# Kernel optimization log

Hardware: AMD Instinct MI355X
Metric: run time of the kernel (lower is better)

The kernel has to match this reference:

```python
import jax, jax.numpy as jnp
import numpy as np

DIM = 4096
N_HEADS = 32
N_KV = 8
HEAD_DIM = DIM // N_HEADS  # 128
ROPE_THETA = 10000.0


def setup_inputs() -> dict:
    key = jax.random.key(0)
    ks = jax.random.split(key, 5)
    B, S = 1, 2048
    x = jax.random.normal(ks[0], (B, S, DIM), jnp.float32)
    wq = jax.random.normal(ks[1], (N_HEADS * HEAD_DIM, DIM), jnp.float32) * 0.02
    wk = jax.random.normal(ks[2], (N_KV * HEAD_DIM, DIM), jnp.float32) * 0.02
    wv = jax.random.normal(ks[3], (N_KV * HEAD_DIM, DIM), jnp.float32) * 0.02
    wo = jax.random.normal(ks[4], (DIM, DIM), jnp.float32) * 0.02
    # precomputed RoPE frequencies: angle[t, i] = t / theta^(2i/head_dim)
    inv_freq = 1.0 / (ROPE_THETA ** (jnp.arange(0, HEAD_DIM, 2, dtype=jnp.float32) / HEAD_DIM))
    t = jnp.arange(S, dtype=jnp.float32)
    angles = jnp.outer(t, inv_freq)  # [S, HEAD_DIM/2]
    return {"x": x, "wq": wq, "wk": wk, "wv": wv, "wo": wo,
            "freqs_cos": jnp.cos(angles), "freqs_sin": jnp.sin(angles)}


def _apply_rope(v, cos, sin):
    # v: [B, S, H, HEAD_DIM]; cos/sin: [S, HEAD_DIM/2]
    # mirrors torch view_as_complex on (..., hd/2, 2): even idx = real, odd idx = imag
    vr = v.reshape(*v.shape[:-1], HEAD_DIM // 2, 2)
    xr, xi = vr[..., 0], vr[..., 1]
    c = cos[None, :, None, :]
    s = sin[None, :, None, :]
    out_r = xr * c - xi * s
    out_i = xr * s + xi * c
    return jnp.stack([out_r, out_i], axis=-1).reshape(v.shape)


def reference(x, wq, wk, wv, wo, freqs_cos, freqs_sin):
    B, S, _ = x.shape
    rep = N_HEADS // N_KV
    q = (x @ wq.T).reshape(B, S, N_HEADS, HEAD_DIM)
    k = (x @ wk.T).reshape(B, S, N_KV, HEAD_DIM)
    v = (x @ wv.T).reshape(B, S, N_KV, HEAD_DIM)
    q = _apply_rope(q, freqs_cos, freqs_sin)
    k = _apply_rope(k, freqs_cos, freqs_sin)
    # native GQA: group query heads per kv head instead of materializing repeated KV
    qg = q.reshape(B, S, N_KV, rep, HEAD_DIM)
    scale = 1.0 / jnp.sqrt(jnp.asarray(HEAD_DIM, jnp.float32))
    scores = jnp.einsum('bqkrd,bskd->bkrqs', qg, k) * scale  # [B, n_kv, rep, S, S]
    causal = jnp.tril(jnp.ones((S, S), bool))
    scores = jnp.where(causal, scores, -jnp.inf)
    probs = jax.nn.softmax(scores, axis=-1)
    out = jnp.einsum('bkrqs,bskd->bqkrd', probs, v).reshape(B, S, DIM)
    return out @ wo.T
```

## Files before the change

### kernel.cpp

```cpp
#include <hip/hip_runtime.h>
#include <cstdint>

typedef __attribute__((ext_vector_type(8))) __bf16 bf16x8;
typedef __attribute__((ext_vector_type(4))) float  f32x4;
typedef __attribute__((ext_vector_type(8))) unsigned short ushort8;

#define DIM 4096
#define SEQ 2048
#define NH  32
#define NKV 8
#define HD  128

__device__ __forceinline__ float b2f(unsigned short u) {
  union { unsigned int i; float f; } v; v.i = ((unsigned int)u) << 16; return v.f;
}
__device__ __forceinline__ unsigned short f2b(float f) {
  union { float f; unsigned int i; } v; v.f = f;
  unsigned int r = v.i + 0x7fffu + ((v.i >> 16) & 1u);
  return (unsigned short)(r >> 16);
}

__device__ __forceinline__ void gl_lds16(const void* g, void* l) {
  __builtin_amdgcn_global_load_lds(
      (const __attribute__((address_space(1))) void*)(uintptr_t)g,
      (__attribute__((address_space(3))) void*)(uintptr_t)l,
      16, 0, 0);
}

__global__ __launch_bounds__(256) void f32_to_bf16(const float* __restrict__ src,
                                                   unsigned short* __restrict__ dst, int n) {
  const int i = (blockIdx.x * 256 + threadIdx.x) * 8;
  if (i >= n) return;
  const float4 a = *(const float4*)(src + i);
  const float4 b = *(const float4*)(src + i + 4);
  ushort8 o;
  o[0] = f2b(a.x); o[1] = f2b(a.y); o[2] = f2b(a.z); o[3] = f2b(a.w);
  o[4] = f2b(b.x); o[5] = f2b(b.y); o[6] = f2b(b.z); o[7] = f2b(b.w);
  *(ushort8*)(dst + i) = o;
}

template <bool OUT_F32>
__global__ __launch_bounds__(256) void gemm_bt(const unsigned short* __restrict__ A,
                                               const unsigned short* __restrict__ B,
                                               void* __restrict__ Cv,
                                               int M, int N, int K) {
  __shared__ __align__(16) unsigned short As[128 * 32];
  __shared__ __align__(16) unsigned short Bs[128 * 32];
  const int n0   = blockIdx.x * 128;
  const int m0   = blockIdx.y * 128;
  const int tid  = threadIdx.x;
  const int w    = tid >> 6;
  const int lane = tid & 63;
  const int quad = lane >> 4;
  const int l15  = lane & 15;
  const int wm   = (w & 1) * 64;
  const int wn   = (w >> 1) * 64;

  const f32x4 fzero = {0.f, 0.f, 0.f, 0.f};
  f32x4 acc[4][4];
#pragma unroll
  for (int i = 0; i < 4; ++i)
#pragma unroll
    for (int j = 0; j < 4; ++j) acc[i][j] = fzero;

  const int srow = lane >> 2;
  const int scol = (lane & 3) * 8;

  for (int k0 = 0; k0 < K; k0 += 32) {
    __syncthreads();
#pragma unroll
    for (int cc = 0; cc < 2; ++cc) {
      const int c   = w * 2 + cc;
      const int row = c * 16 + srow;
      gl_lds16(A + (size_t)(m0 + row) * K + k0 + scol, (char*)As + c * 1024);
      gl_lds16(B + (size_t)(n0 + row) * K + k0 + scol, (char*)Bs + c * 1024);
    }
    __syncthreads();

    bf16x8 af[4], bfr[4];
#pragma unroll
    for (int i = 0; i < 4; ++i) {
      af[i]  = *(const bf16x8*)(As + (wm + i * 16 + l15) * 32 + quad * 8);
      bfr[i] = *(const bf16x8*)(Bs + (wn + i * 16 + l15) * 32 + quad * 8);
    }
#pragma unroll
    for (int i = 0; i < 4; ++i)
#pragma unroll
      for (int j = 0; j < 4; ++j)
        acc[i][j] = __builtin_amdgcn_mfma_f32_16x16x32_bf16(af[i], bfr[j], acc[i][j], 0, 0, 0);
  }

#pragma unroll
  for (int i = 0; i < 4; ++i)
#pragma unroll
    for (int j = 0; j < 4; ++j) {
      const int m = m0 + wm + i * 16 + quad * 4;
      const int n = n0 + wn + j * 16 + l15;
      if (OUT_F32) {
        float* cp = (float*)Cv + (size_t)m * N + n;
#pragma unroll
        for (int r = 0; r < 4; ++r) cp[(size_t)r * N] = acc[i][j][r];
      } else {
        unsigned short* cp = (unsigned short*)Cv + (size_t)m * N + n;
#pragma unroll
        for (int r = 0; r < 4; ++r) cp[(size_t)r * N] = f2b(acc[i][j][r]);
      }
    }
}

template <bool OUT_F32>
__global__ __launch_bounds__(512, 2) void gemm256(const unsigned short* __restrict__ A,
                                                  const unsigned short* __restrict__ B,
                                                  void* __restrict__ Cv,
                                                  int M, int N, int K) {
  __shared__ __align__(16) unsigned short As[2][256 * 64];
  __shared__ __align__(16) unsigned short Bs[2][256 * 64];

  const int n0   = blockIdx.x * 256;
  const int m0   = blockIdx.y * 256;
  const int tid  = threadIdx.x;
  const int w    = tid >> 6;
  const int lane = tid & 63;
  const int quad = lane >> 4;
  const int l15  = lane & 15;
  const int wm   = (w >> 2) * 128;
  const int wn   = (w & 3) * 64;

  const int srow = lane >> 3;
  const int sgr  = (lane & 7) ^ srow;
  const unsigned short* aS = A + (size_t)(m0 + srow) * K + sgr * 8;
  const unsigned short* bS = B + (size_t)(n0 + srow) * K + sgr * 8;

  const int gr0 = ((quad)     ^ (l15 & 7)) * 8;
  const int gr1 = ((quad + 4) ^ (l15 & 7)) * 8;

  const f32x4 fzero = {0.f, 0.f, 0.f, 0.f};
  f32x4 acc[8][4];
#pragma unroll
  for (int i = 0; i < 8; ++i)
#pragma unroll
    for (int j = 0; j < 4; ++j) acc[i][j] = fzero;

  const int NT = K >> 6;

#pragma unroll
  for (int tp = 0; tp < 2; ++tp)
#pragma unroll
    for (int i = 0; i < 4; ++i) {
      const int c = w * 4 + i;
      gl_lds16(aS + (size_t)c * 8 * K + tp * 64, (char*)As[tp] + c * 1024);
      gl_lds16(bS + (size_t)c * 8 * K + tp * 64, (char*)Bs[tp] + c * 1024);
    }

  for (int t = 0; t < NT; ++t) {
    const unsigned short* Ab = As[t & 1] + (wm + l15) * 64;
    const unsigned short* Bb = Bs[t & 1] + (wn + l15) * 64;

    if (t + 2 < NT) asm volatile("s_waitcnt vmcnt(8)" ::: "memory");
    else            asm volatile("s_waitcnt vmcnt(0)" ::: "memory");
    __builtin_amdgcn_s_barrier();
    __builtin_amdgcn_sched_barrier(0);

    bf16x8 af[8][2], bfr[4][2];
#pragma unroll
    for (int mf = 0; mf < 8; ++mf) {
      af[mf][0] = *(const bf16x8*)(Ab + mf * 1024 + gr0);
      af[mf][1] = *(const bf16x8*)(Ab + mf * 1024 + gr1);
    }
#pragma unroll
    for (int nf = 0; nf < 4; ++nf) {
      bfr[nf][0] = *(const bf16x8*)(Bb + nf * 1024 + gr0);
      bfr[nf][1] = *(const bf16x8*)(Bb + nf * 1024 + gr1);
    }

    __builtin_amdgcn_s_setprio(1);
#pragma unroll
    for (int ks = 0; ks < 2; ++ks)
#pragma unroll
      for (int mf = 0; mf < 4; ++mf)
#pragma unroll
        for (int nf = 0; nf < 4; ++nf)
          acc[mf][nf] = __builtin_amdgcn_mfma_f32_16x16x32_bf16(af[mf][ks], bfr[nf][ks],
                                                                acc[mf][nf], 0, 0, 0);
    __builtin_amdgcn_s_setprio(0);

    asm volatile("s_waitcnt lgkmcnt(0)" ::: "memory");
    __builtin_amdgcn_sched_barrier(0);
    __builtin_amdgcn_s_barrier();

    if (t + 2 < NT) {
      const int koff = (t + 2) * 64;
      unsigned short* Ad = As[t & 1];
      unsigned short* Bd = Bs[t & 1];
#pragma unroll
      for (int i = 0; i < 4; ++i) {
        const int c = w * 4 + i;
        gl_lds16(aS + (size_t)c * 8 * K + koff, (char*)Ad + c * 1024);
        gl_lds16(bS + (size_t)c * 8 * K + koff, (char*)Bd + c * 1024);
      }
    }

    __builtin_amdgcn_s_setprio(1);
#pragma unroll
    for (int ks = 0; ks < 2; ++ks)
#pragma unroll
      for (int mf = 4; mf < 8; ++mf)
#pragma unroll
        for (int nf = 0; nf < 4; ++nf)
          acc[mf][nf] = __builtin_amdgcn_mfma_f32_16x16x32_bf16(af[mf][ks], bfr[nf][ks],
                                                                acc[mf][nf], 0, 0, 0);
    __builtin_amdgcn_s_setprio(0);
  }

#pragma unroll
  for (int mf = 0; mf < 8; ++mf)
#pragma unroll
    for (int nf = 0; nf < 4; ++nf) {
      const int m = m0 + wm + mf * 16 + quad * 4;
      const int n = n0 + wn + nf * 16 + l15;
      if (OUT_F32) {
        float* cp = (float*)Cv + (size_t)m * N + n;
#pragma unroll
        for (int r = 0; r < 4; ++r) cp[(size_t)r * N] = acc[mf][nf][r];
      } else {
        unsigned short* cp = (unsigned short*)Cv + (size_t)m * N + n;
#pragma unroll
        for (int r = 0; r < 4; ++r) cp[(size_t)r * N] = f2b(acc[mf][nf][r]);
      }
    }
}

__global__ void rope_kernel(unsigned short* __restrict__ q, int qstride,
                            unsigned short* __restrict__ k, int kstride,
                            const float* __restrict__ Ct, const float* __restrict__ St) {
  const int idx = blockIdx.x * 256 + threadIdx.x;
  const int total = SEQ * (NH * 64 + NKV * 64);
  if (idx >= total) return;
  const int s = idx / 2560;
  const int r = idx - s * 2560;
  unsigned short* base;
  int i;
  if (r < NH * 64) {
    const int h = r >> 6; i = r & 63;
    base = q + (size_t)s * qstride + h * HD + 2 * i;
  } else {
    const int r2 = r - NH * 64; const int h = r2 >> 6; i = r2 & 63;
    base = k + (size_t)s * kstride + h * HD + 2 * i;
  }
  const float c  = Ct[s * 64 + i];
  const float sn = St[s * 64 + i];
  const float xr = b2f(base[0]);
  const float xi = b2f(base[1]);
  base[0] = f2b(xr * c - xi * sn);
  base[1] = f2b(xr * sn + xi * c);
}

__global__ __launch_bounds__(256) void transpose_v(const unsigned short* __restrict__ v,
                                                   int vstride,
                                                   unsigned short* __restrict__ vt) {
  __shared__ unsigned short tile[64][72];
  const int bs = blockIdx.x;
  const int bd = blockIdx.y;
  const int t  = threadIdx.x;
  const int r  = t >> 2;
  const int c0 = (t & 3) * 16;
  const unsigned short* src = v + (size_t)(bs * 64 + r) * vstride + bd * 64 + c0;
#pragma unroll
  for (int i = 0; i < 2; ++i) {
    ushort8 d = *(const ushort8*)(src + i * 8);
#pragma unroll
    for (int e = 0; e < 8; ++e) tile[r][c0 + i * 8 + e] = d[e];
  }
  __syncthreads();
  unsigned short* dst = vt + (size_t)(bd * 64 + r) * SEQ + bs * 64 + c0;
#pragma unroll
  for (int i = 0; i < 2; ++i) {
    ushort8 o;
#pragma unroll
    for (int e = 0; e < 8; ++e) o[e] = tile[c0 + i * 8 + e][r];
    *(ushort8*)(dst + i * 8) = o;
  }
}

__global__ __launch_bounds__(256) void attn_kernel(const unsigned short* __restrict__ Q, int qstride,
                                                   const unsigned short* __restrict__ K, int kstride,
                                                   const unsigned short* __restrict__ VT,
                                                   unsigned short* __restrict__ O) {
  const int bid  = blockIdx.x;
  const int h    = bid & 31;
  const int pr   = bid >> 5;
  const int g    = h >> 2;
  const int tid  = threadIdx.x;
  const int w    = tid >> 6;
  const int lane = tid & 63;
  const int quad = lane >> 4;
  const int l15  = lane & 15;

  __shared__ __align__(16) unsigned short Ks[64 * 128];
  __shared__ __align__(16) unsigned short Vs[128 * 64];
  __shared__ __align__(16) unsigned short Ps[4][32 * 64];

  const float scale = 0.08838834764831845f;
  const f32x4 fzero = {0.f, 0.f, 0.f, 0.f};

  bf16x8 onesf;
#pragma unroll
  for (int e = 0; e < 8; ++e) onesf[e] = (__bf16)1.0f;

  const int ks_row = (lane >> 4);
  const int ks_q   = (lane & 15);
  const int vs_row = (lane >> 3);
  const int vs_q   = (lane & 7) ^ (lane >> 3);

  unsigned short* pw = Ps[w];

  for (int phase = 0; phase < 2; ++phase) {
    const int qt    = phase ? (15 - pr) : pr;
    const int qrow0 = qt * 128 + w * 32;

    bf16x8 qf[2][4];
#pragma unroll
    for (int gq = 0; gq < 2; ++gq) {
      const unsigned short* qb = Q + (size_t)(qrow0 + gq * 16 + l15) * qstride + h * HD + quad * 8;
#pragma unroll
      for (int c = 0; c < 4; ++c) qf[gq][c] = *(const bf16x8*)(qb + c * 32);
    }

    f32x4 oa[2][8];
    f32x4 ls[2];
#pragma unroll
    for (int gq = 0; gq < 2; ++gq) {
      ls[gq] = fzero;
#pragma unroll
      for (int i = 0; i < 8; ++i) oa[gq][i] = fzero;
    }

    const int n_tiles = 2 * qt + 2;

    for (int kt = 0; kt < n_tiles; ++kt) {
      const int kv0 = kt * 64;
      __syncthreads();
#pragma unroll
      for (int cc = 0; cc < 4; ++cc) {
        const int c = w * 4 + cc;
        {
          const int row = c * 4 + ks_row;
          const int qch = ks_q ^ (row & 15);
          gl_lds16(K + (size_t)(kv0 + row) * kstride + g * HD + qch * 8, (char*)Ks + c * 1024);
        }
        {
          const int row = c * 8 + vs_row;
          gl_lds16(VT + (size_t)(g * HD + row) * SEQ + kv0 + vs_q * 8, (char*)Vs + c * 1024);
        }
      }
      __syncthreads();

      f32x4 s[2][4];
#pragma unroll
      for (int gq = 0; gq < 2; ++gq)
#pragma unroll
        for (int ks = 0; ks < 4; ++ks) s[gq][ks] = fzero;
#pragma unroll
      for (int c = 0; c < 4; ++c)
#pragma unroll
        for (int ks = 0; ks < 4; ++ks) {
          const int row = ks * 16 + l15;
          const int p   = (c * 4 + quad) ^ l15;
          bf16x8 kf = *(const bf16x8*)(Ks + row * 128 + p * 8);
          s[0][ks] = __builtin_amdgcn_mfma_f32_16x16x32_bf16(qf[0][c], kf, s[0][ks], 0, 0, 0);
          s[1][ks] = __builtin_amdgcn_mfma_f32_16x16x32_bf16(qf[1][c], kf, s[1][ks], 0, 0, 0);
        }

#pragma unroll
      for (int gq = 0; gq < 2; ++gq)
#pragma unroll
        for (int r = 0; r < 4; ++r) {
          const int qrow = qrow0 + gq * 16 + quad * 4 + r;
          const int prow = gq * 16 + quad * 4 + r;
#pragma unroll
          for (int ks = 0; ks < 4; ++ks) {
            const float ex = __expf(s[gq][ks][r] * scale);
            const float e  = (kv0 + ks * 16 + l15 <= qrow) ? ex : 0.f;
            const int qc = ks * 2 + (l15 >> 3);
            const int p  = qc ^ (prow & 7);
            pw[prow * 64 + p * 8 + (l15 & 7)] = f2b(e);
          }
        }

#pragma unroll
      for (int ki = 0; ki < 2; ++ki) {
        bf16x8 pf[2];
#pragma unroll
        for (int gq = 0; gq < 2; ++gq) {
          const int row = gq * 16 + l15;
          const int p   = (ki * 4 + quad) ^ (l15 & 7);
          pf[gq] = *(const bf16x8*)(pw + row * 64 + p * 8);
        }
        ls[0] = __builtin_amdgcn_mfma_f32_16x16x32_bf16(pf[0], onesf, ls[0], 0, 0, 0);
        ls[1] = __builtin_amdgcn_mfma_f32_16x16x32_bf16(pf[1], onesf, ls[1], 0, 0, 0);
#pragma unroll
        for (int nt = 0; nt < 8; ++nt) {
          const int vrow = nt * 16 + l15;
          const int p    = (ki * 4 + quad) ^ (l15 & 7);
          bf16x8 vf = *(const bf16x8*)(Vs + vrow * 64 + p * 8);
          oa[0][nt] = __builtin_amdgcn_mfma_f32_16x16x32_bf16(pf[0], vf, oa[0][nt], 0, 0, 0);
          oa[1][nt] = __builtin_amdgcn_mfma_f32_16x16x32_bf16(pf[1], vf, oa[1][nt], 0, 0, 0);
        }
      }
    }

#pragma unroll
    for (int gq = 0; gq < 2; ++gq)
#pragma unroll
      for (int r = 0; r < 4; ++r) {
        const float inv = 1.f / ls[gq][r];
        const int qrow = qrow0 + gq * 16 + quad * 4 + r;
        unsigned short* orow = O + (size_t)qrow * DIM + h * HD;
#pragma unroll
        for (int nt = 0; nt < 8; ++nt) orow[nt * 16 + l15] = f2b(oa[gq][nt][r] * inv);
      }
  }
}

extern "C" void kernel_launch(void* const* d_in, const int* in_sizes, int n_in,
                              void* d_out, int out_size, void* d_ws, size_t ws_size,
                              hipStream_t stream) {
  const float* x  = (const float*)d_in[0];
  const float* wq = (const float*)d_in[1];
  const float* wk = (const float*)d_in[2];
  const float* wv = (const float*)d_in[3];
  const float* wo = (const float*)d_in[4];
  const float* fc = (const float*)d_in[5];
  const float* fs = (const float*)d_in[6];
  float* outp = (float*)d_out;

  const dim3 blk(256);
  const size_t M1 = 1024 * 1024;
  const int nx  = SEQ * DIM;
  const int nqw = DIM * DIM;
  const int nkw = NKV * HD * DIM;
  const int total = SEQ * (NH * 64 + NKV * 64);

  const size_t fused_elems = (8 + 24 + 12 + 2 + 8) * M1;

  if (ws_size >= fused_elems * 2) {
    unsigned short* xb   = (unsigned short*)d_ws;
    unsigned short* wbuf = xb   + 8  * M1;
    unsigned short* qkv  = wbuf + 24 * M1;
    unsigned short* vtb  = qkv  + 12 * M1;
    unsigned short* aob  = vtb  + 2  * M1;

    f32_to_bf16<<<dim3(nx  / 2048), blk, 0, stream>>>(x,  xb, nx);
    f32_to_bf16<<<dim3(nqw / 2048), blk, 0, stream>>>(wq, wbuf, nqw);
    f32_to_bf16<<<dim3(nkw / 2048), blk, 0, stream>>>(wk, wbuf + 16 * M1, nkw);
    f32_to_bf16<<<dim3(nkw / 2048), blk, 0, stream>>>(wv, wbuf + 20 * M1, nkw);

    gemm256<false><<<dim3(6144 / 256, SEQ / 256), dim3(512), 0, stream>>>(xb, wbuf, qkv,
                                                                          SEQ, 6144, DIM);

    rope_kernel<<<dim3((total + 255) / 256), blk, 0, stream>>>(qkv, 6144, qkv + 4096, 6144, fc, fs);
    transpose_v<<<dim3(SEQ / 64, 1024 / 64), blk, 0, stream>>>(qkv + 5120, 6144, vtb);
    attn_kernel<<<dim3(256), blk, 0, stream>>>(qkv, 6144, qkv + 4096, 6144, vtb, aob);

    f32_to_bf16<<<dim3(nqw / 2048), blk, 0, stream>>>(wo, wbuf, nqw);
    gemm_bt<true><<<dim3(DIM / 128, SEQ / 128), blk, 0, stream>>>(aob, wbuf, outp, SEQ, DIM, DIM);
  } else {
    unsigned short* xb   = (unsigned short*)d_ws;
    unsigned short* wbuf = xb   + 8  * M1;
    unsigned short* qb   = wbuf + 16 * M1;
    unsigned short* kvb  = qb   + 8  * M1;
    unsigned short* vtb  = kvb  + 4  * M1;
    unsigned short* aob  = vtb  + 2  * M1;

    f32_to_bf16<<<dim3(nx  / 2048), blk, 0, stream>>>(x,  xb, nx);
    f32_to_bf16<<<dim3(nqw / 2048), blk, 0, stream>>>(wq, wbuf, nqw);
    gemm_bt<false><<<dim3(DIM / 128, SEQ / 128), blk, 0, stream>>>(xb, wbuf, qb, SEQ, DIM, DIM);

    f32_to_bf16<<<dim3(nkw / 2048), blk, 0, stream>>>(wk, wbuf, nkw);
    f32_to_bf16<<<dim3(nkw / 2048), blk, 0, stream>>>(wv, wbuf + 4 * M1, nkw);
    gemm_bt<false><<<dim3(2048 / 128, SEQ / 128), blk, 0, stream>>>(xb, wbuf, kvb, SEQ, 2048, DIM);

    rope_kernel<<<dim3((total + 255) / 256), blk, 0, stream>>>(qb, 4096, kvb, 2048, fc, fs);
    transpose_v<<<dim3(SEQ / 64, 1024 / 64), blk, 0, stream>>>(kvb + 1024, 2048, vtb);
    attn_kernel<<<dim3(256), blk, 0, stream>>>(qb, 4096, kvb, 2048, vtb, aob);

    f32_to_bf16<<<dim3(nqw / 2048), blk, 0, stream>>>(wo, wbuf, nqw);
    gemm_bt<true><<<dim3(DIM / 128, SEQ / 128), blk, 0, stream>>>(aob, wbuf, outp, SEQ, DIM, DIM);
  }
}
```

Before: 516.7 us.

## Add 128x256-tile double-buffered GEMM for Q and output projections

Adds a new GEMM kernel with 128x256 tiles and 512 threads that stages tiles into swizzled LDS through direct global-to-LDS loads. It double-buffers across K steps and splits the MFMA work around the prefetch issue so that loads overlap compute. The Q projection and the output projection switch from the 128x128 gemm_bt to this kernel to get more operand reuse per block. The trade-off is fewer blocks (256 for the 2048x4096 output) and more registers and LDS per block, which may hurt occupancy or wave balance.

```diff
diff --git a/kernel.cpp b/kernel.cpp
--- a/kernel.cpp
+++ b/kernel.cpp
@@ -230,6 +230,137 @@
     }
 }
 
+template <bool OUT_F32>
+__global__ __launch_bounds__(512, 2) void gemm128n256(const unsigned short* __restrict__ A,
+                                                      const unsigned short* __restrict__ B,
+                                                      void* __restrict__ Cv,
+                                                      int M, int N, int K) {
+  __shared__ __align__(16) unsigned short As[2][128 * 64];
+  __shared__ __align__(16) unsigned short Bs[2][256 * 64];
+
+  const int n0   = blockIdx.x * 256;
+  const int m0   = blockIdx.y * 128;
+  const int tid  = threadIdx.x;
+  const int w    = tid >> 6;
+  const int lane = tid & 63;
+  const int quad = lane >> 4;
+  const int l15  = lane & 15;
+  const int wm   = (w >> 2) * 64;
+  const int wn   = (w & 3) * 64;
+
+  const int srow = lane >> 3;
+  const int sgr  = (lane & 7) ^ srow;
+  const unsigned short* aS = A + (size_t)(m0 + srow) * K + sgr * 8;
+  const unsigned short* bS = B + (size_t)(n0 + srow) * K + sgr * 8;
+
+  const int gr0 = ((quad)     ^ (l15 & 7)) * 8;
+  const int gr1 = ((quad + 4) ^ (l15 & 7)) * 8;
+
+  const f32x4 fzero = {0.f, 0.f, 0.f, 0.f};
+  f32x4 acc[4][4];
+#pragma unroll
+  for (int i = 0; i < 4; ++i)
+#pragma unroll
+    for (int j = 0; j < 4; ++j) acc[i][j] = fzero;
+
+  const int NT = K >> 6;
+
+#pragma unroll
+  for (int tp = 0; tp < 2; ++tp) {
+#pragma unroll
+    for (int i = 0; i < 2; ++i) {
+      const int c = w * 2 + i;
+      gl_lds16(aS + (size_t)c * 8 * K + tp * 64, (char*)As[tp] + c * 1024);
+    }
+#pragma unroll
+    for (int i = 0; i < 4; ++i) {
+      const int c = w * 4 + i;
+      gl_lds16(bS + (size_t)c * 8 * K + tp * 64, (char*)Bs[tp] + c * 1024);
+    }
+  }
+
+  for (int t = 0; t < NT; ++t) {
+    const unsigned short* Ab = As[t & 1] + (wm + l15) * 64;
+    const unsigned short* Bb = Bs[t & 1] + (wn + l15) * 64;
+
+    if (t + 2 < NT) asm volatile("s_waitcnt vmcnt(6)" ::: "memory");
+    else            asm volatile("s_waitcnt vmcnt(0)" ::: "memory");
+    __builtin_amdgcn_s_barrier();
+    __builtin_amdgcn_sched_barrier(0);
+
+    bf16x8 af[4][2], bfr[4][2];
+#pragma unroll
+    for (int mf = 0; mf < 4; ++mf) {
+      af[mf][0] = *(const bf16x8*)(Ab + mf * 1024 + gr0);
+      af[mf][1] = *(const bf16x8*)(Ab + mf * 1024 + gr1);
+    }
+#pragma unroll
+    for (int nf = 0; nf < 4; ++nf) {
+      bfr[nf][0] = *(const bf16x8*)(Bb + nf * 1024 + gr0);
+      bfr[nf][1] = *(const bf16x8*)(Bb + nf * 1024 + gr1);
+    }
+
+    __builtin_amdgcn_s_setprio(1);
+#pragma unroll
+    for (int ks = 0; ks < 2; ++ks)
+#pragma unroll
+      for (int mf = 0; mf < 2; ++mf)
+#pragma unroll
+        for (int nf = 0; nf < 4; ++nf)
+          acc[mf][nf] = __builtin_amdgcn_mfma_f32_16x16x32_bf16(af[mf][ks], bfr[nf][ks],
+                                                                acc[mf][nf], 0, 0, 0);
+    __builtin_amdgcn_s_setprio(0);
+
+    asm volatile("s_waitcnt lgkmcnt(0)" ::: "memory");
+    __builtin_amdgcn_sched_barrier(0);
+    __builtin_amdgcn_s_barrier();
+
+    if (t + 2 < NT) {
+      const int koff = (t + 2) * 64;
+      unsigned short* Ad = As[t & 1];
+      unsigned short* Bd = Bs[t & 1];
+#pragma unroll
+      for (int i = 0; i < 2; ++i) {
+        const int c = w * 2 + i;
+        gl_lds16(aS + (size_t)c * 8 * K + koff, (char*)Ad + c * 1024);
+      }
+#pragma unroll
+      for (int i = 0; i < 4; ++i) {
+        const int c = w * 4 + i;
+        gl_lds16(bS + (size_t)c * 8 * K + koff, (char*)Bd + c * 1024);
+      }
+    }
+
+    __builtin_amdgcn_s_setprio(1);
+#pragma unroll
+    for (int ks = 0; ks < 2; ++ks)
+#pragma unroll
+      for (int mf = 2; mf < 4; ++mf)
+#pragma unroll
+        for (int nf = 0; nf < 4; ++nf)
+          acc[mf][nf] = __builtin_amdgcn_mfma_f32_16x16x32_bf16(af[mf][ks], bfr[nf][ks],
+                                                                acc[mf][nf], 0, 0, 0);
+    __builtin_amdgcn_s_setprio(0);
+  }
+
+#pragma unroll
+  for (int mf = 0; mf < 4; ++mf)
+#pragma unroll
+    for (int nf = 0; nf < 4; ++nf) {
+      const int m = m0 + wm + mf * 16 + quad * 4;
+      const int n = n0 + wn + nf * 16 + l15;
+      if (OUT_F32) {
+        float* cp = (float*)Cv + (size_t)m * N + n;
+#pragma unroll
+        for (int r = 0; r < 4; ++r) cp[(size_t)r * N] = acc[mf][nf][r];
+      } else {
+        unsigned short* cp = (unsigned short*)Cv + (size_t)m * N + n;
+#pragma unroll
+        for (int r = 0; r < 4; ++r) cp[(size_t)r * N] = f2b(acc[mf][nf][r]);
+      }
+    }
+}
+
 __global__ void rope_kernel(unsigned short* __restrict__ q, int qstride,
                             unsigned short* __restrict__ k, int kstride,
                             const float* __restrict__ Ct, const float* __restrict__ St) {
@@ -463,7 +594,8 @@
     attn_kernel<<<dim3(256), blk, 0, stream>>>(qkv, 6144, qkv + 4096, 6144, vtb, aob);
 
     f32_to_bf16<<<dim3(nqw / 2048), blk, 0, stream>>>(wo, wbuf, nqw);
-    gemm_bt<true><<<dim3(DIM / 128, SEQ / 128), blk, 0, stream>>>(aob, wbuf, outp, SEQ, DIM, DIM);
+    gemm128n256<true><<<dim3(DIM / 256, SEQ / 128), dim3(512), 0, stream>>>(aob, wbuf, outp,
+                                                                            SEQ, DIM, DIM);
   } else {
     unsigned short* xb   = (unsigned short*)d_ws;
     unsigned short* wbuf = xb   + 8  * M1;
@@ -474,7 +606,8 @@
 
     f32_to_bf16<<<dim3(nx  / 2048), blk, 0, stream>>>(x,  xb, nx);
     f32_to_bf16<<<dim3(nqw / 2048), blk, 0, stream>>>(wq, wbuf, nqw);
-    gemm_bt<false><<<dim3(DIM / 128, SEQ / 128), blk, 0, stream>>>(xb, wbuf, qb, SEQ, DIM, DIM);
+    gemm128n256<false><<<dim3(DIM / 256, SEQ / 128), dim3(512), 0, stream>>>(xb, wbuf, qb,
+                                                                             SEQ, DIM, DIM);
 
     f32_to_bf16<<<dim3(nkw / 2048), blk, 0, stream>>>(wk, wbuf, nkw);
     f32_to_bf16<<<dim3(nkw / 2048), blk, 0, stream>>>(wv, wbuf + 4 * M1, nkw);
@@ -485,6 +618,7 @@
     attn_kernel<<<dim3(256), blk, 0, stream>>>(qb, 4096, kvb, 2048, vtb, aob);
 
     f32_to_bf16<<<dim3(nqw / 2048), blk, 0, stream>>>(wo, wbuf, nqw);
-    gemm_bt<true><<<dim3(DIM / 128, SEQ / 128), blk, 0, stream>>>(aob, wbuf, outp, SEQ, DIM, DIM);
-  }
-}
+    gemm128n256<true><<<dim3(DIM / 256, SEQ / 128), dim3(512), 0, stream>>>(aob, wbuf, outp,
+                                                                            SEQ, DIM, DIM);
+  }
+}
```

Result: faster. 476.1 us (-7.9%).

## Replace 256x256 GEMM with templated 128xNF*64 tile GEMM for QKV and output

Applied to the files above, without the earlier changes.

The 256x256 GEMM becomes a templated kernel with 128-row tiles and a configurable N width (192 for the fused QKV projection, 128 for the output projection). The per-iteration pipeline is reworked to one barrier per K-step, and the next tile is prefetched only one step ahead. The goal is more workgroups in flight (occupancy hint 4) and better CU fill for 2048x6144 and 2048x4096. In exchange, each tile gets less data reuse, the prefetch runs shallower, and the new kernel also replaces the older gemm_bt path for the output projection.

```diff
diff --git a/kernel.cpp b/kernel.cpp
--- a/kernel.cpp
+++ b/kernel.cpp
@@ -108,23 +108,23 @@
     }
 }
 
-template <bool OUT_F32>
-__global__ __launch_bounds__(512, 2) void gemm256(const unsigned short* __restrict__ A,
+template <int NF, bool OUT_F32>
+__global__ __launch_bounds__(512, 4) void gemm128(const unsigned short* __restrict__ A,
                                                   const unsigned short* __restrict__ B,
                                                   void* __restrict__ Cv,
                                                   int M, int N, int K) {
-  __shared__ __align__(16) unsigned short As[2][256 * 64];
-  __shared__ __align__(16) unsigned short Bs[2][256 * 64];
-
-  const int n0   = blockIdx.x * 256;
-  const int m0   = blockIdx.y * 256;
+  __shared__ __align__(16) unsigned short As[2][128 * 64];
+  __shared__ __align__(16) unsigned short Bs[2][NF * 64 * 64];
+
+  const int n0   = blockIdx.x * (NF * 64);
+  const int m0   = blockIdx.y * 128;
   const int tid  = threadIdx.x;
   const int w    = tid >> 6;
   const int lane = tid & 63;
   const int quad = lane >> 4;
   const int l15  = lane & 15;
-  const int wm   = (w >> 2) * 128;
-  const int wn   = (w & 3) * 64;
+  const int wm   = (w >> 2) * 64;
+  const int wn   = (w & 3) * (NF * 16);
 
   const int srow = lane >> 3;
   const int sgr  = (lane & 7) ^ srow;
@@ -135,87 +135,80 @@
   const int gr1 = ((quad + 4) ^ (l15 & 7)) * 8;
 
   const f32x4 fzero = {0.f, 0.f, 0.f, 0.f};
-  f32x4 acc[8][4];
-#pragma unroll
-  for (int i = 0; i < 8; ++i)
-#pragma unroll
-    for (int j = 0; j < 4; ++j) acc[i][j] = fzero;
+  f32x4 acc[4][NF];
+#pragma unroll
+  for (int i = 0; i < 4; ++i)
+#pragma unroll
+    for (int j = 0; j < NF; ++j) acc[i][j] = fzero;
 
   const int NT = K >> 6;
 
 #pragma unroll
-  for (int tp = 0; tp < 2; ++tp)
-#pragma unroll
-    for (int i = 0; i < 4; ++i) {
-      const int c = w * 4 + i;
-      gl_lds16(aS + (size_t)c * 8 * K + tp * 64, (char*)As[tp] + c * 1024);
-      gl_lds16(bS + (size_t)c * 8 * K + tp * 64, (char*)Bs[tp] + c * 1024);
-    }
+  for (int i = 0; i < 2; ++i) {
+    const int c = w * 2 + i;
+    gl_lds16(aS + (size_t)c * 8 * K, (char*)As[0] + c * 1024);
+  }
+#pragma unroll
+  for (int i = 0; i < NF; ++i) {
+    const int c = w * NF + i;
+    gl_lds16(bS + (size_t)c * 8 * K, (char*)Bs[0] + c * 1024);
+  }
 
   for (int t = 0; t < NT; ++t) {
     const unsigned short* Ab = As[t & 1] + (wm + l15) * 64;
     const unsigned short* Bb = Bs[t & 1] + (wn + l15) * 64;
 
-    if (t + 2 < NT) asm volatile("s_waitcnt vmcnt(8)" ::: "memory");
-    else            asm volatile("s_waitcnt vmcnt(0)" ::: "memory");
+    asm volatile("s_waitcnt vmcnt(0) lgkmcnt(0)" ::: "memory");
     __builtin_amdgcn_s_barrier();
     __builtin_amdgcn_sched_barrier(0);
 
-    bf16x8 af[8][2], bfr[4][2];
-#pragma unroll
-    for (int mf = 0; mf < 8; ++mf) {
-      af[mf][0] = *(const bf16x8*)(Ab + mf * 1024 + gr0);
-      af[mf][1] = *(const bf16x8*)(Ab + mf * 1024 + gr1);
-    }
-#pragma unroll
-    for (int nf = 0; nf < 4; ++nf) {
+    if (t + 1 < NT) {
+      const int koff = (t + 1) * 64;
+      unsigned short* Ad = As[(t + 1) & 1];
+      unsigned short* Bd = Bs[(t + 1) & 1];
+#pragma unroll
+      for (int i = 0; i < 2; ++i) {
+        const int c = w * 2 + i;
+        gl_lds16(aS + (size_t)c * 8 * K + koff, (char*)Ad + c * 1024);
+      }
+#pragma unroll
+      for (int i = 0; i < NF; ++i) {
+        const int c = w * NF + i;
+        gl_lds16(bS + (size_t)c * 8 * K + koff, (char*)Bd + c * 1024);
+      }
+    }
+
+    bf16x8 bfr[NF][2];
+#pragma unroll
+    for (int nf = 0; nf < NF; ++nf) {
       bfr[nf][0] = *(const bf16x8*)(Bb + nf * 1024 + gr0);
       bfr[nf][1] = *(const bf16x8*)(Bb + nf * 1024 + gr1);
     }
-
-    __builtin_amdgcn_s_setprio(1);
-#pragma unroll
-    for (int ks = 0; ks < 2; ++ks)
-#pragma unroll
-      for (int mf = 0; mf < 4; ++mf)
-#pragma unroll
-        for (int nf = 0; nf < 4; ++nf)
-          acc[mf][nf] = __builtin_amdgcn_mfma_f32_16x16x32_bf16(af[mf][ks], bfr[nf][ks],
-                                                                acc[mf][nf], 0, 0, 0);
-    __builtin_amdgcn_s_setprio(0);
-
-    asm volatile("s_waitcnt lgkmcnt(0)" ::: "memory");
-    __builtin_amdgcn_sched_barrier(0);
-    __builtin_amdgcn_s_barrier();
-
-    if (t + 2 < NT) {
-      const int koff = (t + 2) * 64;
-      unsigned short* Ad = As[t & 1];
-      unsigned short* Bd = Bs[t & 1];
-#pragma unroll
-      for (int i = 0; i < 4; ++i) {
-        const int c = w * 4 + i;
-        gl_lds16(aS + (size_t)c * 8 * K + koff, (char*)Ad + c * 1024);
-        gl_lds16(bS + (size_t)c * 8 * K + koff, (char*)Bd + c * 1024);
-      }
-    }
-
-    __builtin_amdgcn_s_setprio(1);
-#pragma unroll
-    for (int ks = 0; ks < 2; ++ks)
-#pragma unroll
-      for (int mf = 4; mf < 8; ++mf)
-#pragma unroll
-        for (int nf = 0; nf < 4; ++nf)
-          acc[mf][nf] = __builtin_amdgcn_mfma_f32_16x16x32_bf16(af[mf][ks], bfr[nf][ks],
-                                                                acc[mf][nf], 0, 0, 0);
-    __builtin_amdgcn_s_setprio(0);
-  }
-
-#pragma unroll
-  for (int mf = 0; mf < 8; ++mf)
-#pragma unroll
-    for (int nf = 0; nf < 4; ++nf) {
+#pragma unroll
+    for (int mp = 0; mp < 2; ++mp) {
+      bf16x8 a0[2], a1[2];
+      a0[0] = *(const bf16x8*)(Ab + (mp * 2 + 0) * 1024 + gr0);
+      a0[1] = *(const bf16x8*)(Ab + (mp * 2 + 0) * 1024 + gr1);
+      a1[0] = *(const bf16x8*)(Ab + (mp * 2 + 1) * 1024 + gr0);
+      a1[1] = *(const bf16x8*)(Ab + (mp * 2 + 1) * 1024 + gr1);
+      __builtin_amdgcn_s_setprio(1);
+#pragma unroll
+      for (int ks = 0; ks < 2; ++ks)
+#pragma unroll
+        for (int nf = 0; nf < NF; ++nf) {
+          acc[mp * 2 + 0][nf] = __builtin_amdgcn_mfma_f32_16x16x32_bf16(a0[ks], bfr[nf][ks],
+                                                                        acc[mp * 2 + 0][nf], 0, 0, 0);
+          acc[mp * 2 + 1][nf] = __builtin_amdgcn_mfma_f32_16x16x32_bf16(a1[ks], bfr[nf][ks],
+                                                                        acc[mp * 2 + 1][nf], 0, 0, 0);
+        }
+      __builtin_amdgcn_s_setprio(0);
+    }
+  }
+
+#pragma unroll
+  for (int mf = 0; mf < 4; ++mf)
+#pragma unroll
+    for (int nf = 0; nf < NF; ++nf) {
       const int m = m0 + wm + mf * 16 + quad * 4;
       const int n = n0 + wn + nf * 16 + l15;
       if (OUT_F32) {
@@ -455,15 +448,16 @@
     f32_to_bf16<<<dim3(nkw / 2048), blk, 0, stream>>>(wk, wbuf + 16 * M1, nkw);
     f32_to_bf16<<<dim3(nkw / 2048), blk, 0, stream>>>(wv, wbuf + 20 * M1, nkw);
 
-    gemm256<false><<<dim3(6144 / 256, SEQ / 256), dim3(512), 0, stream>>>(xb, wbuf, qkv,
-                                                                          SEQ, 6144, DIM);
+    gemm128<3, false><<<dim3(6144 / 192, SEQ / 128), dim3(512), 0, stream>>>(xb, wbuf, qkv,
+                                                                             SEQ, 6144, DIM);
 
     rope_kernel<<<dim3((total + 255) / 256), blk, 0, stream>>>(qkv, 6144, qkv + 4096, 6144, fc, fs);
     transpose_v<<<dim3(SEQ / 64, 1024 / 64), blk, 0, stream>>>(qkv + 5120, 6144, vtb);
     attn_kernel<<<dim3(256), blk, 0, stream>>>(qkv, 6144, qkv + 4096, 6144, vtb, aob);
 
     f32_to_bf16<<<dim3(nqw / 2048), blk, 0, stream>>>(wo, wbuf, nqw);
-    gemm_bt<true><<<dim3(DIM / 128, SEQ / 128), blk, 0, stream>>>(aob, wbuf, outp, SEQ, DIM, DIM);
+    gemm128<2, true><<<dim3(DIM / 128, SEQ / 128), dim3(512), 0, stream>>>(aob, wbuf, outp,
+                                                                           SEQ, DIM, DIM);
   } else {
     unsigned short* xb   = (unsigned short*)d_ws;
     unsigned short* wbuf = xb   + 8  * M1;
@@ -474,7 +468,8 @@
 
     f32_to_bf16<<<dim3(nx  / 2048), blk, 0, stream>>>(x,  xb, nx);
     f32_to_bf16<<<dim3(nqw / 2048), blk, 0, stream>>>(wq, wbuf, nqw);
-    gemm_bt<false><<<dim3(DIM / 128, SEQ / 128), blk, 0, stream>>>(xb, wbuf, qb, SEQ, DIM, DIM);
+    gemm128<2, false><<<dim3(DIM / 128, SEQ / 128), dim3(512), 0, stream>>>(xb, wbuf, qb,
+                                                                            SEQ, DIM, DIM);
 
     f32_to_bf16<<<dim3(nkw / 2048), blk, 0, stream>>>(wk, wbuf, nkw);
     f32_to_bf16<<<dim3(nkw / 2048), blk, 0, stream>>>(wv, wbuf + 4 * M1, nkw);
@@ -485,6 +480,7 @@
     attn_kernel<<<dim3(256), blk, 0, stream>>>(qb, 4096, kvb, 2048, vtb, aob);
 
     f32_to_bf16<<<dim3(nqw / 2048), blk, 0, stream>>>(wo, wbuf, nqw);
-    gemm_bt<true><<<dim3(DIM / 128, SEQ / 128), blk, 0, stream>>>(aob, wbuf, outp, SEQ, DIM, DIM);
-  }
-}
+    gemm128<2, true><<<dim3(DIM / 128, SEQ / 128), dim3(512), 0, stream>>>(aob, wbuf, outp,
+                                                                           SEQ, DIM, DIM);
+  }
+}
```

New measurement: 467.6 us. 9.5% less time.
